# Optimization experiments

Measured on AMD Instinct MI355X. Metric: run time of the kernel, lower is better.

Reference implementation:

```python
import jax, jax.numpy as jnp
import numpy as np
from jax import lax

DIM = 256
POS = 32
RATIO = 4
LN_EPS = 1e-5


def _layernorm(x, g, b):
    m = x.mean(-1, keepdims=True)
    v = ((x - m) ** 2).mean(-1, keepdims=True)
    return (x - m) * lax.rsqrt(v + LN_EPS) * g + b


def _pos_embed(pos, h, w):
    # pos: [1, C, POS, POS] -> bilinear (align_corners=False / half-pixel) -> [1, h*w, C]
    p = jax.image.resize(pos, (1, pos.shape[1], h, w), method='bilinear')
    return p.transpose(0, 2, 3, 1).reshape(1, h * w, pos.shape[1])


def _scan_branch(u, ln_g, ln_b, Wf, bf, Ww, bw, Wo, bo):
    # u: [B, N, C]. Pooled LN context -> concat gates -> gated linear recurrence.
    c = _layernorm(u.mean(1), ln_g, ln_b)                       # [B, C]
    z = jnp.concatenate([u, jnp.broadcast_to(c[:, None, :], u.shape)], -1)
    d = jax.nn.softplus(z @ Wf + bf)
    g = jax.nn.sigmoid(z @ Ww + bw)
    o = jax.nn.sigmoid(z @ Wo + bo)
    a = jnp.exp(-d)
    b = (1.0 - a) * (g * u)

    def step(s, t):
        a_t, b_t, o_t, u_t = t
        s = a_t * s + b_t
        return s, o_t * s + (1.0 - o_t) * u_t

    xs = tuple(jnp.swapaxes(v, 0, 1) for v in (a, b, o, u))     # [N, B, C]
    s0 = jnp.zeros((u.shape[0], u.shape[2]), u.dtype)
    _, y = lax.scan(step, s0, xs)
    return jnp.swapaxes(y, 0, 1)                                # [B, N, C]


def setup_inputs() -> dict:
    key = jax.random.key(0)
    ks = jax.random.split(key, 32)
    d = DIM

    def W(k, i, o, s=0.02):
        return (jax.random.normal(k, (i, o), jnp.float32) * s)

    inp = {
        'x': jax.random.normal(ks[0], (8, d, 64, 64), jnp.float32),
        'Wt': W(ks[1], d, d), 'bt': jnp.zeros((d,), jnp.float32),
        'pos_fine': jax.random.normal(ks[2], (1, d, POS, POS), jnp.float32) * 0.02,
        'pos_glob': jax.random.normal(ks[3], (1, d, POS, POS), jnp.float32) * 0.02,
        'ln_g': jnp.ones((d,), jnp.float32), 'ln_b': jnp.zeros((d,), jnp.float32),
        'Wf': W(ks[4], 2 * d, d), 'bf': jnp.zeros((d,), jnp.float32),
        'Ww': W(ks[5], 2 * d, d), 'bw': jnp.zeros((d,), jnp.float32),
        'Wo': W(ks[6], 2 * d, d), 'bo': jnp.zeros((d,), jnp.float32),
        'Wr': W(ks[7], 3 * d, d), 'br': jnp.zeros((d,), jnp.float32),
        'Wgi': W(ks[8], 3 * d, d), 'bgi': jnp.zeros((d,), jnp.float32),
        'dw_w': jax.random.normal(ks[9], (d, 1, 3, 3), jnp.float32) * 0.1,
        'dw_b': jnp.zeros((d,), jnp.float32),
        'Wl': W(ks[10], d, d), 'bl': jnp.zeros((d,), jnp.float32),
        'Wlf': W(ks[11], 2 * d, d), 'blf': jnp.zeros((d,), jnp.float32),
        'Wout': W(ks[12], d, d), 'bout': jnp.zeros((d,), jnp.float32),
    }
    return inp


def reference(x, Wt, bt, pos_fine, pos_glob, ln_g, ln_b, Wf, bf, Ww, bw, Wo, bo,
              Wr, br, Wgi, bgi, dw_w, dw_b, Wl, bl, Wlf, blf, Wout, bout):
    bsz, c, h, w = x.shape
    gate_params = (ln_g, ln_b, Wf, bf, Ww, bw, Wo, bo)

    # fine sequence: token proj + interpolated learnable pos
    seq = x.transpose(0, 2, 3, 1).reshape(bsz, h * w, c)
    u = seq @ Wt + bt + _pos_embed(pos_fine, h, w)

    # bidirectional gated scan
    y_f = _scan_branch(u, *gate_params)
    y_b = jnp.flip(_scan_branch(jnp.flip(u, 1), *gate_params), 1)
    rho = jax.nn.sigmoid(jnp.concatenate([u, y_f, y_b], -1) @ Wr + br)
    y = rho * y_f + (1.0 - rho) * y_b

    # global branch: exact avg pool (H,W divisible by RATIO) -> scan -> upsample
    gh, gw = h // RATIO, w // RATIO
    x_g = x.reshape(bsz, c, gh, RATIO, gw, RATIO).mean((3, 5))
    seq_g = x_g.transpose(0, 2, 3, 1).reshape(bsz, gh * gw, c)
    u_g = seq_g @ Wt + bt + _pos_embed(pos_glob, gh, gw)
    y_g = _scan_branch(u_g, *gate_params)
    y_g_map = y_g.reshape(bsz, gh, gw, c).transpose(0, 3, 1, 2)
    y_g_up = jax.image.resize(y_g_map, (bsz, c, h, w), method='bilinear')
    y_g_seq = y_g_up.transpose(0, 2, 3, 1).reshape(bsz, h * w, c)

    lam = jax.nn.sigmoid(jnp.concatenate([y, y_g_seq, u], -1) @ Wgi + bgi)
    z = y + lam * y_g_seq

    # local depthwise conv branch
    v_map = lax.conv_general_dilated(x, dw_w, (1, 1), 'SAME',
                                     feature_group_count=c) + dw_b[None, :, None, None]
    v = v_map.transpose(0, 2, 3, 1).reshape(bsz, h * w, c) @ Wl + bl
    eta = jax.nn.sigmoid(jnp.concatenate([v, z], -1) @ Wlf + blf)
    u_out = eta * v + (1.0 - eta) * z

    # 1x1 conv output proj + residual
    out_map = (u_out @ Wout + bout).reshape(bsz, h, w, c).transpose(0, 3, 1, 2)
    return x + out_map
```

## Files before the change

kernel.cpp:

```cpp
#include <hip/hip_runtime.h>
#include <cstddef>

#define B_  8
#define C_  256
#define H_  64
#define W_  64
#define HW_ 4096
#define NG_ 256

typedef unsigned short u16;
typedef __attribute__((ext_vector_type(8))) short short8;
typedef __attribute__((ext_vector_type(4))) float f32x4;

__device__ __forceinline__ float sigm(float v) { return 1.f / (1.f + expf(-v)); }

__device__ __forceinline__ u16 f2bf(float f) {
    union { float f; unsigned u; } x; x.f = f;
    unsigned r = x.u + 0x7fff + ((x.u >> 16) & 1);
    return (u16)(r >> 16);
}
__device__ __forceinline__ float bf2f(u16 h) {
    union { unsigned u; float f; } x; x.u = ((unsigned)h) << 16;
    return x.f;
}

__global__ __launch_bounds__(256) void prepw_k(
    const float* __restrict__ Wt, const float* __restrict__ Wf, const float* __restrict__ Ww,
    const float* __restrict__ Wo, const float* __restrict__ Wr, const float* __restrict__ Wgi,
    const float* __restrict__ Wl, const float* __restrict__ Wlf, const float* __restrict__ Wout,
    u16* __restrict__ Wpre)
{
    int s = blockIdx.z;
    const float* Wsrc; int rowoff = 0;
    switch (s) {
        case 0: Wsrc = Wt; break;
        case 1: Wsrc = Wf; break;
        case 2: Wsrc = Ww; break;
        case 3: Wsrc = Wo; break;
        case 4: case 5: case 6: Wsrc = Wr;  rowoff = (s - 4) * 256; break;
        case 7: case 8: case 9: Wsrc = Wgi; rowoff = (s - 7) * 256; break;
        case 10: Wsrc = Wl; break;
        case 11: case 12: Wsrc = Wlf; rowoff = (s - 11) * 256; break;
        default: Wsrc = Wout; break;
    }
    __shared__ float t[32][33];
    int k0 = blockIdx.y * 32, n0 = blockIdx.x * 32;
    int tx = threadIdx.x, ty = threadIdx.y;
#pragma unroll
    for (int i = 0; i < 32; i += 8)
        t[ty + i][tx] = Wsrc[(size_t)(rowoff + k0 + ty + i) * 256 + n0 + tx];
    __syncthreads();
    u16* op = Wpre + (size_t)s * 65536;
#pragma unroll
    for (int i = 0; i < 32; i += 8)
        op[(size_t)(n0 + ty + i) * 256 + k0 + tx] = f2bf(t[tx][ty + i]);
}

#define SWZ(row, qoff) ((row) * 128 + ((qoff) ^ (((row) & 7) << 4)))

__global__ __launch_bounds__(256, 4) void gemm_bf16(
    const u16* __restrict__ A0, const u16* __restrict__ A1, const u16* __restrict__ A2,
    int nseg, const u16* __restrict__ Wpre, const float* __restrict__ bias,
    const float* __restrict__ pos, const float* __restrict__ aux0,
    const u16* __restrict__ auxb0, const u16* __restrict__ auxb1,
    float* __restrict__ out, u16* __restrict__ out2, int NTOK, int mode)
{
    __shared__ u16 Asm[64 * 64];
    __shared__ u16 Bsm[128 * 64];
    const int tid = threadIdx.x;
    const int lane = tid & 63, wave = tid >> 6;
    const int wm = wave & 1, wn = wave >> 1;
    const int m0 = blockIdx.x * 64, n0 = blockIdx.y * 128;
    const int l15 = lane & 15, lq = lane >> 4;

    f32x4 acc[2][4] = {};

    const int rowS = tid >> 3, colS = tid & 7;

    short8 av[2], bv[4];
    {
        av[0] = *(const short8*)(A0 + (size_t)(m0 + rowS) * 256 + colS * 8);
        av[1] = *(const short8*)(A0 + (size_t)(m0 + 32 + rowS) * 256 + colS * 8);
#pragma unroll
        for (int i = 0; i < 4; ++i)
            bv[i] = *(const short8*)(Wpre + (size_t)(n0 + i * 32 + rowS) * 256 + colS * 8);
    }

    const int nq = nseg * 4;
    for (int q = 0; q < nq; ++q) {
        __syncthreads();
        *(short8*)((char*)Asm + SWZ(rowS,      colS * 16)) = av[0];
        *(short8*)((char*)Asm + SWZ(rowS + 32, colS * 16)) = av[1];
#pragma unroll
        for (int i = 0; i < 4; ++i)
            *(short8*)((char*)Bsm + SWZ(i * 32 + rowS, colS * 16)) = bv[i];

        if (q + 1 < nq) {
            const int q1 = q + 1, seg = q1 >> 2, k0 = (q1 & 3) << 6;
            const u16* __restrict__ A = (seg == 0) ? A0 : ((seg == 1) ? A1 : A2);
            const u16* __restrict__ Wq = Wpre + (size_t)seg * 65536;
            av[0] = *(const short8*)(A + (size_t)(m0 + rowS) * 256 + k0 + colS * 8);
            av[1] = *(const short8*)(A + (size_t)(m0 + 32 + rowS) * 256 + k0 + colS * 8);
#pragma unroll
            for (int i = 0; i < 4; ++i)
                bv[i] = *(const short8*)(Wq + (size_t)(n0 + i * 32 + rowS) * 256 + k0 + colS * 8);
        }
        __syncthreads();

#pragma unroll
        for (int ks = 0; ks < 2; ++ks) {
            short8 af[2], bfr[4];
#pragma unroll
            for (int i = 0; i < 2; ++i) {
                const int row = wm * 32 + i * 16 + l15;
                af[i] = *(const short8*)((char*)Asm + SWZ(row, ks * 64 + lq * 16));
            }
#pragma unroll
            for (int j = 0; j < 4; ++j) {
                const int row = wn * 64 + j * 16 + l15;
                bfr[j] = *(const short8*)((char*)Bsm + SWZ(row, ks * 64 + lq * 16));
            }
#pragma unroll
            for (int i = 0; i < 2; ++i)
#pragma unroll
                for (int j = 0; j < 4; ++j)
                    acc[i][j] = __builtin_amdgcn_mfma_f32_16x16x32_bf16(
                        af[i], bfr[j], acc[i][j], 0, 0, 0);
        }
    }

#pragma unroll
    for (int i = 0; i < 2; ++i) {
        int mbase = m0 + wm * 32 + i * 16 + lq * 4;
#pragma unroll
        for (int j = 0; j < 4; ++j) {
            int n = n0 + wn * 64 + j * 16 + l15;
            if (mode == 9) {
                int b9 = mbase >> 12, hw = mbase & 4095;
                size_t oi = ((size_t)b9 * 256 + n) * 4096 + hw;
                float bn = bias[n];
                float4 xr = *(const float4*)(aux0 + oi);
                float4 res;
                res.x = xr.x + acc[i][j][0] + bn;
                res.y = xr.y + acc[i][j][1] + bn;
                res.z = xr.z + acc[i][j][2] + bn;
                res.w = xr.w + acc[i][j][3] + bn;
                *(float4*)(out + oi) = res;
                continue;
            }
            float bn = bias[n];
#pragma unroll
            for (int r = 0; r < 4; ++r) {
                int m = mbase + r;
                size_t idx = (size_t)m * 256 + n;
                float D = acc[i][j][r] + bn;
                if (mode == 1) {
                    float v = D + pos[(size_t)(m % NTOK) * 256 + n];
                    out[idx] = v; out2[idx] = f2bf(v);
                } else if (mode == 10) {
                    float v = D + pos[(size_t)(m % NTOK) * 256 + n];
                    out2[idx] = f2bf(v);
                } else if (mode == 11) {
                    float r_ = sigm(D);
                    out2[idx] = f2bf(r_ * bf2f(auxb0[idx]) + (1.f - r_) * bf2f(auxb1[idx]));
                } else if (mode == 6) {
                    float l = sigm(D);
                    out2[idx] = f2bf(bf2f(auxb1[idx]) + l * bf2f(auxb0[idx]));
                } else if (mode == 7) {
                    out2[idx] = f2bf(D);
                } else {
                    float e = sigm(D);
                    out2[idx] = f2bf(e * bf2f(auxb0[idx]) + (1.f - e) * bf2f(auxb1[idx]));
                }
            }
        }
    }
}

#define LDK 72
__global__ __launch_bounds__(256, 4) void gemm_gates3(
    const u16* __restrict__ A0, const u16* __restrict__ Wg, const float* __restrict__ cf,
    const u16* __restrict__ ubf, float* __restrict__ aF, float* __restrict__ bbF,
    u16* __restrict__ obf, int NTOK)
{
    __shared__ u16 Asm[64 * LDK];
    __shared__ u16 Bsm3[3][64 * LDK];
    const int tid = threadIdx.x;
    const int lane = tid & 63, wave = tid >> 6;
    const int wm = wave & 1, wn = wave >> 1;
    const int m0 = blockIdx.x * 64, n0 = blockIdx.y * 64;
    const int l15 = lane & 15, lq = lane >> 4;

    f32x4 acc[3][2][2] = {};

    const int rowA = tid >> 2, kA = (tid & 3) * 16;
    const u16* arow = A0 + (size_t)(m0 + rowA) * 256 + kA;
    const u16* wrow = Wg + (size_t)(n0 + rowA) * 256 + kA;

    for (int k0 = 0; k0 < 256; k0 += 64) {
        *(short8*)(&Asm[rowA * LDK + kA])     = *(const short8*)(arow + k0);
        *(short8*)(&Asm[rowA * LDK + kA + 8]) = *(const short8*)(arow + k0 + 8);
#pragma unroll
        for (int ws = 0; ws < 3; ++ws) {
            const u16* wr = wrow + (size_t)ws * 65536 + k0;
            *(short8*)(&Bsm3[ws][rowA * LDK + kA])     = *(const short8*)(wr);
            *(short8*)(&Bsm3[ws][rowA * LDK + kA + 8]) = *(const short8*)(wr + 8);
        }
        __syncthreads();
#pragma unroll
        for (int ks = 0; ks < 2; ++ks) {
            short8 af[2];
#pragma unroll
            for (int i = 0; i < 2; ++i)
                af[i] = *(const short8*)(&Asm[(wm * 32 + i * 16 + l15) * LDK + ks * 32 + lq * 8]);
#pragma unroll
            for (int ws = 0; ws < 3; ++ws) {
                short8 bfr[2];
#pragma unroll
                for (int j = 0; j < 2; ++j)
                    bfr[j] = *(const short8*)(&Bsm3[ws][(wn * 32 + j * 16 + l15) * LDK + ks * 32 + lq * 8]);
#pragma unroll
                for (int i = 0; i < 2; ++i)
#pragma unroll
                    for (int j = 0; j < 2; ++j)
                        acc[ws][i][j] = __builtin_amdgcn_mfma_f32_16x16x32_bf16(
                            af[i], bfr[j], acc[ws][i][j], 0, 0, 0);
            }
        }
        __syncthreads();
    }

#pragma unroll
    for (int i = 0; i < 2; ++i) {
        int mbase = m0 + wm * 32 + i * 16 + lq * 4;
        int bt_ = mbase / NTOK;
#pragma unroll
        for (int j = 0; j < 2; ++j) {
            int n = n0 + wn * 32 + j * 16 + l15;
            float cD = cf[((size_t)0 * B_ + bt_) * C_ + n];
            float cW = cf[((size_t)1 * B_ + bt_) * C_ + n];
            float cO = cf[((size_t)2 * B_ + bt_) * C_ + n];
#pragma unroll
            for (int r = 0; r < 4; ++r) {
                size_t idx = (size_t)(mbase + r) * 256 + n;
                float a_ = sigm(-(acc[0][i][j][r] + cD));
                float g_ = sigm(acc[1][i][j][r] + cW);
                float o_ = sigm(acc[2][i][j][r] + cO);
                float u_ = bf2f(ubf[idx]);
                aF[idx]  = a_;
                bbF[idx] = (1.f - a_) * g_ * u_;
                obf[idx] = f2bf(o_);
            }
        }
    }
}

__global__ __launch_bounds__(256) void transpose_bf_k(const float* __restrict__ in,
                                                      u16* __restrict__ outb)
{
    __shared__ float t[32][33];
    int b = blockIdx.z;
    int r0 = blockIdx.y * 32, c0 = blockIdx.x * 32;
    int tx = threadIdx.x, ty = threadIdx.y;
    const float* ip = in + (size_t)b * HW_ * C_;
    u16* op = outb + (size_t)b * HW_ * C_;
#pragma unroll
    for (int k = 0; k < 32; k += 8)
        t[ty + k][tx] = ip[(size_t)(r0 + ty + k) * HW_ + c0 + tx];
    __syncthreads();
#pragma unroll
    for (int k = 0; k < 32; k += 8)
        op[(size_t)(c0 + ty + k) * C_ + r0 + tx] = f2bf(t[tx][ty + k]);
}

__global__ __launch_bounds__(256) void dwconvt3_k(const float* __restrict__ x,
                                                  const float* __restrict__ dww,
                                                  const float* __restrict__ dwb,
                                                  u16* __restrict__ vseq)
{
    __shared__ float sx[32 * 384];
    __shared__ float sw[32 * 9];
    __shared__ float sb[32];
    const int t = threadIdx.x;
    const int l   = (blockIdx.x & 7) * 128 + (blockIdx.x >> 3);
    const int hch = l & 15;
    const int chb = (l >> 4) & 7;
    const int b   = l >> 7;
    const int r0 = chb * 32, h0 = hch * 4;

    for (int p = t; p < 288; p += 256) sw[p] = dww[(size_t)(r0 + p / 9) * 9 + p % 9];
    if (t < 32) sb[t] = dwb[r0 + t];

    const float* xb = x + (size_t)(b * 256 + r0) * 4096;
#pragma unroll
    for (int j = 0; j < 12; ++j) {
        int seg = j * 256 + t;
        int ch  = seg / 96;
        int r4  = seg - ch * 96;
        int rr  = r4 >> 4;
        int w4  = (r4 & 15) * 4;
        int hh  = h0 - 1 + rr;
        float4 v = make_float4(0.f, 0.f, 0.f, 0.f);
        if (hh >= 0 && hh <= 63)
            v = *(const float4*)(xb + (size_t)ch * 4096 + hh * 64 + w4);
        *(float4*)(&sx[seg * 4]) = v;
    }
    __syncthreads();

    const int w = t & 63, chq = t >> 6;
    float res[4][8];
#pragma unroll
    for (int i = 0; i < 8; ++i) {
        const int ch = chq * 8 + i;
        const float* cw = &sw[ch * 9];
        const float* bp = &sx[ch * 384 + w];
        float aa[4];
        aa[0] = aa[1] = aa[2] = aa[3] = sb[ch];
#pragma unroll
        for (int rr = 0; rr < 6; ++rr) {
            const float* rp = bp + rr * 64;
            float cc = rp[0];
            float lf = (w > 0)  ? rp[-1] : 0.f;
            float rt = (w < 63) ? rp[1]  : 0.f;
            if (rr < 4)            aa[rr]     += lf * cw[0] + cc * cw[1] + rt * cw[2];
            if (rr >= 1 && rr < 5) aa[rr - 1] += lf * cw[3] + cc * cw[4] + rt * cw[5];
            if (rr >= 2)           aa[rr - 2] += lf * cw[6] + cc * cw[7] + rt * cw[8];
        }
#pragma unroll
        for (int r = 0; r < 4; ++r) res[r][i] = aa[r];
    }

    size_t obase = ((size_t)b * HW_ + (size_t)(h0 * 64 + w)) * 256 + r0 + chq * 8;
#pragma unroll
    for (int r = 0; r < 4; ++r) {
        short8 v;
#pragma unroll
        for (int i = 0; i < 8; ++i) v[i] = (short)f2bf(res[r][i]);
        *(short8*)(vseq + obase + (size_t)r * 64 * 256) = v;
    }
}

__global__ __launch_bounds__(256) void pool_k(const float* __restrict__ x, u16* __restrict__ seqg)
{
    int b = blockIdx.x, c = blockIdx.y, ghw = threadIdx.x;
    int gh = ghw >> 4, gw = ghw & 15;
    const float* xp = x + ((size_t)b * C_ + c) * HW_;
    float s = 0.f;
#pragma unroll
    for (int dy = 0; dy < 4; ++dy)
#pragma unroll
        for (int dx = 0; dx < 4; ++dx)
            s += xp[(gh * 4 + dy) * W_ + gw * 4 + dx];
    seqg[((size_t)b * NG_ + ghw) * C_ + c] = f2bf(s * (1.f / 16.f));
}

__global__ __launch_bounds__(256) void posfine_k(const float* __restrict__ pf, float* __restrict__ posF)
{
    int hw = blockIdx.x, c = threadIdx.x;
    int h = hw >> 6, w = hw & 63;
    float fy = h * 0.5f - 0.25f, fx = w * 0.5f - 0.25f;
    int y0 = (int)floorf(fy); float wy = fy - (float)y0;
    int x0 = (int)floorf(fx); float wx = fx - (float)x0;
    int y0c = min(max(y0, 0), 31), y1c = min(max(y0 + 1, 0), 31);
    int x0c = min(max(x0, 0), 31), x1c = min(max(x0 + 1, 0), 31);
    const float* p = pf + (size_t)c * 1024;
    float v = (1.f - wy) * ((1.f - wx) * p[y0c * 32 + x0c] + wx * p[y0c * 32 + x1c])
            +        wy  * ((1.f - wx) * p[y1c * 32 + x0c] + wx * p[y1c * 32 + x1c]);
    posF[(size_t)hw * C_ + c] = v;
}

__global__ __launch_bounds__(256) void posglob_k(const float* __restrict__ pg, float* __restrict__ posG)
{
    int ghw = blockIdx.x, c = threadIdx.x;
    int gh = ghw >> 4, gw = ghw & 15;
    const float wt[4] = {0.125f, 0.375f, 0.375f, 0.125f};
    float wy[4], wx[4]; int jy[4], jx[4];
    float sy = 0.f, sx = 0.f;
#pragma unroll
    for (int k = 0; k < 4; ++k) {
        jy[k] = 2 * gh - 1 + k; jx[k] = 2 * gw - 1 + k;
        wy[k] = (jy[k] >= 0 && jy[k] < 32) ? wt[k] : 0.f; sy += wy[k];
        wx[k] = (jx[k] >= 0 && jx[k] < 32) ? wt[k] : 0.f; sx += wx[k];
    }
    const float* p = pg + (size_t)c * 1024;
    float acc = 0.f;
#pragma unroll
    for (int ky = 0; ky < 4; ++ky) {
        if (wy[ky] == 0.f) continue;
        float row = 0.f;
#pragma unroll
        for (int kx = 0; kx < 4; ++kx)
            if (wx[kx] != 0.f) row += wx[kx] * p[jy[ky] * 32 + jx[kx]];
        acc += wy[ky] * row;
    }
    posG[(size_t)ghw * C_ + c] = acc / (sy * sx);
}

__global__ __launch_bounds__(256) void upsample_k(const float* __restrict__ yg, u16* __restrict__ ygs)
{
    int b = blockIdx.x >> 12, hw = blockIdx.x & 4095, c = threadIdx.x;
    int h = hw >> 6, w = hw & 63;
    float fy = h * 0.25f - 0.375f, fx = w * 0.25f - 0.375f;
    int y0 = (int)floorf(fy); float wy = fy - (float)y0;
    int x0 = (int)floorf(fx); float wx = fx - (float)x0;
    int y0c = min(max(y0, 0), 15), y1c = min(max(y0 + 1, 0), 15);
    int x0c = min(max(x0, 0), 15), x1c = min(max(x0 + 1, 0), 15);
    const float* p = yg + (size_t)b * NG_ * C_ + c;
    float v = (1.f - wy) * ((1.f - wx) * p[(y0c * 16 + x0c) * C_] + wx * p[(y0c * 16 + x1c) * C_])
            +        wy  * ((1.f - wx) * p[(y1c * 16 + x0c) * C_] + wx * p[(y1c * 16 + x1c) * C_]);
    ygs[((size_t)b * HW_ + hw) * C_ + c] = f2bf(v);
}

__global__ __launch_bounds__(256) void meanpart_k(const float* __restrict__ u, float* __restrict__ part,
                                                  int Ntok, int chunkLen)
{
    int b = blockIdx.x, s = blockIdx.y, c = threadIdx.x;
    float acc = 0.f;
    for (int i = 0; i < chunkLen; ++i) {
        int t = s * chunkLen + i;
        acc += u[((size_t)b * Ntok + t) * C_ + c];
    }
    part[((size_t)b * gridDim.y + s) * C_ + c] = acc;
}

__global__ __launch_bounds__(256) void meanpart_bf_k(const u16* __restrict__ u, float* __restrict__ part,
                                                     int Ntok, int chunkLen)
{
    int b = blockIdx.x, s = blockIdx.y, c = threadIdx.x;
    float acc = 0.f;
    for (int i = 0; i < chunkLen; ++i) {
        int t = s * chunkLen + i;
        acc += bf2f(u[((size_t)b * Ntok + t) * C_ + c]);
    }
    part[((size_t)b * gridDim.y + s) * C_ + c] = acc;
}

__global__ __launch_bounds__(256) void ln_k(const float* __restrict__ part, int S, float invN,
                                            const float* __restrict__ g, const float* __restrict__ bta,
                                            float* __restrict__ cout)
{
    __shared__ float red[256];
    int c = threadIdx.x, b = blockIdx.x;
    float v = 0.f;
    for (int s = 0; s < S; ++s) v += part[((size_t)b * S + s) * C_ + c];
    v *= invN;
    red[c] = v; __syncthreads();
    for (int st = 128; st > 0; st >>= 1) { if (c < st) red[c] += red[c + st]; __syncthreads(); }
    float m = red[0] * (1.f / 256.f);
    __syncthreads();
    float d = v - m;
    red[c] = d * d; __syncthreads();
    for (int st = 128; st > 0; st >>= 1) { if (c < st) red[c] += red[c + st]; __syncthreads(); }
    float var = red[0] * (1.f / 256.f);
    cout[(size_t)b * C_ + c] = d * rsqrtf(var + 1e-5f) * g[c] + bta[c];
}

__global__ __launch_bounds__(256) void gatebias_k(const float* __restrict__ cvec,
    const float* __restrict__ Wf, const float* __restrict__ bf,
    const float* __restrict__ Ww, const float* __restrict__ bw,
    const float* __restrict__ Wo, const float* __restrict__ bo,
    float* __restrict__ outb)
{
    int n = threadIdx.x, b = blockIdx.x, gate = blockIdx.y;
    const float* Wm = (gate == 0) ? Wf : ((gate == 1) ? Ww : Wo);
    const float* bi = (gate == 0) ? bf : ((gate == 1) ? bw : bo);
    __shared__ float cs[256];
    cs[n] = cvec[(size_t)b * C_ + n];
    __syncthreads();
    float acc = bi[n];
    for (int k = 0; k < 256; ++k)
        acc += cs[k] * Wm[(size_t)(256 + k) * C_ + n];
    outb[((size_t)gate * B_ + b) * C_ + n] = acc;
}

__global__ __launch_bounds__(256) void scan_p1b(
    const float* __restrict__ a, const float* __restrict__ bb,
    float* __restrict__ AbF, float* __restrict__ BbF,
    float* __restrict__ AbB, float* __restrict__ BbB,
    int Ntok, int nchunk, int both)
{
    int c = threadIdx.x;
    int ch = blockIdx.x % nchunk;
    int b = blockIdx.x / nchunk;
    int CL = Ntok / nchunk;
    size_t base = ((size_t)b * Ntok + (size_t)ch * CL) * C_ + c;
    float sA = 1.f, sB = 0.f;
    for (int i = 0; i < CL; ++i) {
        float av = a[base + (size_t)i * C_];
        sB = av * sB + bb[base + (size_t)i * C_];
        sA *= av;
    }
    size_t o = ((size_t)b * nchunk + ch) * C_ + c;
    AbF[o] = sA; BbF[o] = sB;
    if (both) {
        sA = 1.f; sB = 0.f;
        for (int i = CL - 1; i >= 0; --i) {
            float av = a[base + (size_t)i * C_];
            sB = av * sB + bb[base + (size_t)i * C_];
            sA *= av;
        }
        size_t ob = ((size_t)b * nchunk + (nchunk - 1 - ch)) * C_ + c;
        AbB[ob] = sA; BbB[ob] = sB;
    }
}

__global__ __launch_bounds__(512) void scan_p2c(
    const float* __restrict__ AbF, const float* __restrict__ BbF, float* __restrict__ SbF,
    const float* __restrict__ AbB, const float* __restrict__ BbB, float* __restrict__ SbB,
    int nchunk, int both)
{
    const int c = threadIdx.x & 255, half = threadIdx.x >> 8, b = blockIdx.x;
    if (half && !both) return;
    const float* __restrict__ Ap = half ? AbB : AbF;
    const float* __restrict__ Bp = half ? BbB : BbF;
    float* __restrict__       Sp = half ? SbB : SbF;
    const size_t base = (size_t)b * nchunk * C_ + c;
    float a0[8], b0[8], a1[8], b1[8];
#pragma unroll
    for (int j = 0; j < 8; ++j) {
        a0[j] = Ap[base + (size_t)j * C_];
        b0[j] = Bp[base + (size_t)j * C_];
    }
    float s = 0.f;
    const int nb = nchunk >> 3;
    for (int t = 0; t < nb; ++t) {
        const size_t nbase = base + (size_t)(t + 1) * 8 * C_;
        if (t + 1 < nb) {
#pragma unroll
            for (int j = 0; j < 8; ++j) {
                a1[j] = Ap[nbase + (size_t)j * C_];
                b1[j] = Bp[nbase + (size_t)j * C_];
            }
        }
        const size_t cbase = base + (size_t)t * 8 * C_;
#pragma unroll
        for (int j = 0; j < 8; ++j) {
            Sp[cbase + (size_t)j * C_] = s;
            s = a0[j] * s + b0[j];
        }
#pragma unroll
        for (int j = 0; j < 8; ++j) { a0[j] = a1[j]; b0[j] = b1[j]; }
    }
}

__global__ __launch_bounds__(256) void scan_p3b(
    const float* __restrict__ a, const float* __restrict__ bb,
    const u16* __restrict__ obf, const u16* __restrict__ ubf,
    const float* __restrict__ SbF, const float* __restrict__ SbB,
    float* __restrict__ yout, u16* __restrict__ ybfF, u16* __restrict__ ybfB,
    int Ntok, int nchunk, int both)
{
    int c = threadIdx.x;
    int ch = blockIdx.x % nchunk;
    int b = blockIdx.x / nchunk;
    int CL = Ntok / nchunk;
    size_t base = ((size_t)b * Ntok + (size_t)ch * CL) * C_ + c;
    float s = SbF[((size_t)b * nchunk + ch) * C_ + c];
    for (int i = 0; i < CL; ++i) {
        size_t idx = base + (size_t)i * C_;
        float av = a[idx];
        s = av * s + bb[idx];
        float ov = bf2f(obf[idx]);
        float y = ov * s + (1.f - ov) * bf2f(ubf[idx]);
        if (yout) yout[idx] = y;
        if (ybfF) ybfF[idx] = f2bf(y);
    }
    if (both) {
        float sb = SbB[((size_t)b * nchunk + (nchunk - 1 - ch)) * C_ + c];
        for (int i = CL - 1; i >= 0; --i) {
            size_t idx = base + (size_t)i * C_;
            float av = a[idx];
            sb = av * sb + bb[idx];
            float ov = bf2f(obf[idx]);
            ybfB[idx] = f2bf(ov * sb + (1.f - ov) * bf2f(ubf[idx]));
        }
    }
}

extern "C" void kernel_launch(void* const* d_in, const int* in_sizes, int n_in,
                              void* d_out, int out_size, void* d_ws, size_t ws_size,
                              hipStream_t stream)
{
    const float* x        = (const float*)d_in[0];
    const float* Wt       = (const float*)d_in[1];
    const float* bt       = (const float*)d_in[2];
    const float* pos_fine = (const float*)d_in[3];
    const float* pos_glob = (const float*)d_in[4];
    const float* ln_g     = (const float*)d_in[5];
    const float* ln_b     = (const float*)d_in[6];
    const float* Wf       = (const float*)d_in[7];
    const float* bf       = (const float*)d_in[8];
    const float* Ww       = (const float*)d_in[9];
    const float* bw       = (const float*)d_in[10];
    const float* Wo       = (const float*)d_in[11];
    const float* bo       = (const float*)d_in[12];
    const float* Wr       = (const float*)d_in[13];
    const float* br       = (const float*)d_in[14];
    const float* Wgi      = (const float*)d_in[15];
    const float* bgi      = (const float*)d_in[16];
    const float* dww      = (const float*)d_in[17];
    const float* dwb      = (const float*)d_in[18];
    const float* Wl       = (const float*)d_in[19];
    const float* bl       = (const float*)d_in[20];
    const float* Wlf      = (const float*)d_in[21];
    const float* blf      = (const float*)d_in[22];
    const float* Wout     = (const float*)d_in[23];
    const float* bout     = (const float*)d_in[24];
    float* out = (float*)d_out;

    float* w = (float*)d_ws;
    const size_t BNC = (size_t)B_ * HW_ * C_;
    float* bu  = w + 0 * BNC;
    float* ba  = w + 1 * BNC;
    float* bbb = w + 2 * BNC;
    float* bo_ = w + 3 * BNC;
    u16* bf1 = (u16*)(w + 4 * BNC);
    u16* bf2 = bf1 + BNC;
    u16* bf3 = bf2 + BNC;
    u16* bf4 = bf3 + BNC;
    u16* bf5 = bf4 + BNC;
    float* ext = w + 4 * BNC + 5 * (BNC / 2);
    float* posF = ext;  ext += (size_t)HW_ * C_;
    float* posG = ext;  ext += (size_t)NG_ * C_;
    float* part = ext;  ext += (size_t)B_ * 32 * C_;
    float* cln  = ext;  ext += (size_t)B_ * C_;
    float* cf   = ext;  ext += (size_t)3 * B_ * C_;
    float* ug   = ext;  ext += (size_t)B_ * NG_ * C_;
    float* ag   = ext;  ext += (size_t)B_ * NG_ * C_;
    float* bbg  = ext;  ext += (size_t)B_ * NG_ * C_;
    float* ygt  = ext;  ext += (size_t)B_ * NG_ * C_;
    u16* seqg_bf = (u16*)ext;  ext += (size_t)B_ * NG_ * C_ / 2;
    u16* ug_bf   = (u16*)ext;  ext += (size_t)B_ * NG_ * C_ / 2;
    u16* og_bf   = (u16*)ext;  ext += (size_t)B_ * NG_ * C_ / 2;
    u16* Wpre    = (u16*)ext;
    const size_t CHS = (size_t)B_ * 256 * C_;
    float* chAF = bu + 0 * CHS;
    float* chBF = bu + 1 * CHS;
    float* chSF = bu + 2 * CHS;
    float* chAB = bu + 3 * CHS;
    float* chBB = bu + 4 * CHS;
    float* chSB = bu + 5 * CHS;
    u16* obf    = (u16*)bo_;

    const dim3 blk256(256);
    const dim3 blkT(32, 8);
    const dim3 gBig(B_ * HW_ / 64, 2);
    const dim3 gSml(B_ * NG_ / 64, 2);
    const dim3 gGateF(B_ * HW_ / 64, 4);
    const dim3 gGateG(B_ * NG_ / 64, 4);
    const size_t WS = 65536;
    const int NCH_F = 256;
    const int NCH_G = 16;
    const float *F0 = nullptr; const u16 *U0 = nullptr;
    float *FW = nullptr; u16 *UW = nullptr;

    prepw_k<<<dim3(8, 8, 14), blkT, 0, stream>>>(Wt, Wf, Ww, Wo, Wr, Wgi, Wl, Wlf, Wout, Wpre);

    transpose_bf_k<<<dim3(HW_ / 32, C_ / 32, B_), blkT, 0, stream>>>(x, bf1);
    posfine_k<<<HW_, blk256, 0, stream>>>(pos_fine, posF);
    gemm_bf16<<<gBig, blk256, 0, stream>>>(bf1, U0, U0, 1, Wpre + 0 * WS, bt,
        posF, F0, U0, U0, FW, bf2, HW_, 10);

    pool_k<<<dim3(B_, C_), blk256, 0, stream>>>(x, seqg_bf);
    posglob_k<<<NG_, blk256, 0, stream>>>(pos_glob, posG);
    gemm_bf16<<<gSml, blk256, 0, stream>>>(seqg_bf, U0, U0, 1, Wpre + 0 * WS, bt,
        posG, F0, U0, U0, ug, ug_bf, NG_, 1);
    meanpart_k<<<dim3(B_, 8), blk256, 0, stream>>>(ug, part, NG_, 32);
    ln_k<<<B_, blk256, 0, stream>>>(part, 8, 1.f / NG_, ln_g, ln_b, cln);
    gatebias_k<<<dim3(B_, 3), blk256, 0, stream>>>(cln, Wf, bf, Ww, bw, Wo, bo, cf);
    gemm_gates3<<<gGateG, blk256, 0, stream>>>(ug_bf, Wpre + 1 * WS, cf, ug_bf,
        ag, bbg, og_bf, NG_);
    scan_p1b<<<B_ * NCH_G, blk256, 0, stream>>>(ag, bbg, chAF, chBF, FW, FW, NG_, NCH_G, 0);
    scan_p2c<<<B_, dim3(512), 0, stream>>>(chAF, chBF, chSF, F0, F0, FW, NCH_G, 0);
    scan_p3b<<<B_ * NCH_G, blk256, 0, stream>>>(ag, bbg, og_bf, ug_bf, chSF, F0,
        ygt, UW, UW, NG_, NCH_G, 0);
    upsample_k<<<B_ * HW_, blk256, 0, stream>>>(ygt, bf5);

    meanpart_bf_k<<<dim3(B_, 32), blk256, 0, stream>>>(bf2, part, HW_, 128);
    ln_k<<<B_, blk256, 0, stream>>>(part, 32, 1.f / HW_, ln_g, ln_b, cln);
    gatebias_k<<<dim3(B_, 3), blk256, 0, stream>>>(cln, Wf, bf, Ww, bw, Wo, bo, cf);
    gemm_gates3<<<gGateF, blk256, 0, stream>>>(bf2, Wpre + 1 * WS, cf, bf2,
        ba, bbb, obf, HW_);
    scan_p1b<<<B_ * NCH_F, blk256, 0, stream>>>(ba, bbb, chAF, chBF, chAB, chBB, HW_, NCH_F, 1);
    scan_p2c<<<B_, dim3(512), 0, stream>>>(chAF, chBF, chSF, chAB, chBB, chSB, NCH_F, 1);
    scan_p3b<<<B_ * NCH_F, blk256, 0, stream>>>(ba, bbb, obf, bf2, chSF, chSB,
        FW, bf1, bf3, HW_, NCH_F, 1);

    gemm_bf16<<<gBig, blk256, 0, stream>>>(bf2, bf1, bf3, 3, Wpre + 4 * WS, br,
        F0, F0, bf1, bf3, FW, bf4, HW_, 11);

    gemm_bf16<<<gBig, blk256, 0, stream>>>(bf4, bf5, bf2, 3, Wpre + 7 * WS, bgi,
        F0, F0, bf5, bf4, FW, bf1, HW_, 6);

    dwconvt3_k<<<dim3(1024), blk256, 0, stream>>>(x, dww, dwb, bf3);
    gemm_bf16<<<gBig, blk256, 0, stream>>>(bf3, U0, U0, 1, Wpre + 10 * WS, bl,
        F0, F0, U0, U0, FW, bf2, HW_, 7);
    gemm_bf16<<<gBig, blk256, 0, stream>>>(bf2, bf1, U0, 2, Wpre + 11 * WS, blf,
        F0, F0, bf2, bf1, FW, bf3, HW_, 8);

    gemm_bf16<<<gBig, blk256, 0, stream>>>(bf3, U0, U0, 1, Wpre + 13 * WS, bout,
        F0, x, U0, U0, out, UW, HW_, 9);
}
```

Baseline: 568.4 us.

## Fuse chunk-scan phase 1 into gates GEMM epilogue and swizzle LDS tiles

The first pass of the chunked scan, which computed per-chunk (A,B) summaries, is folded into the gates GEMM epilogue. Each 16-row tile is reduced with a register prefix and lane shuffles, for both forward and backward directions, so the separate scan_p1b kernel and its re-read of a/b from global memory go away. The GEMM's shared-memory staging also switches from padded rows to a swizzled layout, with register prefetch of the next k-slice. This assumes 16-token chunks (NCH = NTOK/16), which must match what scan_p2c/p3b expect, and it adds shuffle work to the epilogue.

```diff
diff --git a/kernel.cpp b/kernel.cpp
--- a/kernel.cpp
+++ b/kernel.cpp
@@ -177,14 +177,16 @@
     }
 }
 
-#define LDK 72
 __global__ __launch_bounds__(256, 4) void gemm_gates3(
     const u16* __restrict__ A0, const u16* __restrict__ Wg, const float* __restrict__ cf,
     const u16* __restrict__ ubf, float* __restrict__ aF, float* __restrict__ bbF,
-    u16* __restrict__ obf, int NTOK)
-{
-    __shared__ u16 Asm[64 * LDK];
-    __shared__ u16 Bsm3[3][64 * LDK];
+    u16* __restrict__ obf,
+    float* __restrict__ chAF, float* __restrict__ chBF,
+    float* __restrict__ chAB, float* __restrict__ chBB,
+    int NTOK, int both)
+{
+    __shared__ u16 Asm[64 * 64];
+    __shared__ u16 Bsm3[3][64 * 64];
     const int tid = threadIdx.x;
     const int lane = tid & 63, wave = tid >> 6;
     const int wm = wave & 1, wn = wave >> 1;
@@ -193,32 +195,58 @@
 
     f32x4 acc[3][2][2] = {};
 
-    const int rowA = tid >> 2, kA = (tid & 3) * 16;
-    const u16* arow = A0 + (size_t)(m0 + rowA) * 256 + kA;
-    const u16* wrow = Wg + (size_t)(n0 + rowA) * 256 + kA;
-
-    for (int k0 = 0; k0 < 256; k0 += 64) {
-        *(short8*)(&Asm[rowA * LDK + kA])     = *(const short8*)(arow + k0);
-        *(short8*)(&Asm[rowA * LDK + kA + 8]) = *(const short8*)(arow + k0 + 8);
+    const int rowS = tid >> 3, colS = tid & 7;
+
+    short8 av[2], bv[3][2];
+    {
+        av[0] = *(const short8*)(A0 + (size_t)(m0 + rowS) * 256 + colS * 8);
+        av[1] = *(const short8*)(A0 + (size_t)(m0 + 32 + rowS) * 256 + colS * 8);
 #pragma unroll
         for (int ws = 0; ws < 3; ++ws) {
-            const u16* wr = wrow + (size_t)ws * 65536 + k0;
-            *(short8*)(&Bsm3[ws][rowA * LDK + kA])     = *(const short8*)(wr);
-            *(short8*)(&Bsm3[ws][rowA * LDK + kA + 8]) = *(const short8*)(wr + 8);
-        }
+            const u16* wp = Wg + (size_t)ws * 65536;
+            bv[ws][0] = *(const short8*)(wp + (size_t)(n0 + rowS) * 256 + colS * 8);
+            bv[ws][1] = *(const short8*)(wp + (size_t)(n0 + 32 + rowS) * 256 + colS * 8);
+        }
+    }
+
+    for (int q = 0; q < 4; ++q) {
         __syncthreads();
+        *(short8*)((char*)Asm + SWZ(rowS,      colS * 16)) = av[0];
+        *(short8*)((char*)Asm + SWZ(rowS + 32, colS * 16)) = av[1];
+#pragma unroll
+        for (int ws = 0; ws < 3; ++ws) {
+            *(short8*)((char*)Bsm3[ws] + SWZ(rowS,      colS * 16)) = bv[ws][0];
+            *(short8*)((char*)Bsm3[ws] + SWZ(rowS + 32, colS * 16)) = bv[ws][1];
+        }
+        if (q < 3) {
+            const int k0 = (q + 1) << 6;
+            av[0] = *(const short8*)(A0 + (size_t)(m0 + rowS) * 256 + k0 + colS * 8);
+            av[1] = *(const short8*)(A0 + (size_t)(m0 + 32 + rowS) * 256 + k0 + colS * 8);
+#pragma unroll
+            for (int ws = 0; ws < 3; ++ws) {
+                const u16* wp = Wg + (size_t)ws * 65536;
+                bv[ws][0] = *(const short8*)(wp + (size_t)(n0 + rowS) * 256 + k0 + colS * 8);
+                bv[ws][1] = *(const short8*)(wp + (size_t)(n0 + 32 + rowS) * 256 + k0 + colS * 8);
+            }
+        }
+        __syncthreads();
+
 #pragma unroll
         for (int ks = 0; ks < 2; ++ks) {
             short8 af[2];
 #pragma unroll
-            for (int i = 0; i < 2; ++i)
-                af[i] = *(const short8*)(&Asm[(wm * 32 + i * 16 + l15) * LDK + ks * 32 + lq * 8]);
+            for (int i = 0; i < 2; ++i) {
+                const int row = wm * 32 + i * 16 + l15;
+                af[i] = *(const short8*)((char*)Asm + SWZ(row, ks * 64 + lq * 16));
+            }
 #pragma unroll
             for (int ws = 0; ws < 3; ++ws) {
                 short8 bfr[2];
 #pragma unroll
-                for (int j = 0; j < 2; ++j)
-                    bfr[j] = *(const short8*)(&Bsm3[ws][(wn * 32 + j * 16 + l15) * LDK + ks * 32 + lq * 8]);
+                for (int j = 0; j < 2; ++j) {
+                    const int row = wn * 32 + j * 16 + l15;
+                    bfr[j] = *(const short8*)((char*)Bsm3[ws] + SWZ(row, ks * 64 + lq * 16));
+                }
 #pragma unroll
                 for (int i = 0; i < 2; ++i)
 #pragma unroll
@@ -227,19 +255,21 @@
                             af[i], bfr[j], acc[ws][i][j], 0, 0, 0);
             }
         }
-        __syncthreads();
-    }
-
+    }
+
+    const int nch = NTOK >> 4;
 #pragma unroll
     for (int i = 0; i < 2; ++i) {
-        int mbase = m0 + wm * 32 + i * 16 + lq * 4;
-        int bt_ = mbase / NTOK;
+        const int mtile = m0 + wm * 32 + i * 16;
+        const int mbase = mtile + lq * 4;
+        const int bt_ = mbase / NTOK;
 #pragma unroll
         for (int j = 0; j < 2; ++j) {
             int n = n0 + wn * 32 + j * 16 + l15;
             float cD = cf[((size_t)0 * B_ + bt_) * C_ + n];
             float cW = cf[((size_t)1 * B_ + bt_) * C_ + n];
             float cO = cf[((size_t)2 * B_ + bt_) * C_ + n];
+            float a4[4], b4[4];
 #pragma unroll
             for (int r = 0; r < 4; ++r) {
                 size_t idx = (size_t)(mbase + r) * 256 + n;
@@ -247,9 +277,48 @@
                 float g_ = sigm(acc[1][i][j][r] + cW);
                 float o_ = sigm(acc[2][i][j][r] + cO);
                 float u_ = bf2f(ubf[idx]);
+                float b_ = (1.f - a_) * g_ * u_;
                 aF[idx]  = a_;
-                bbF[idx] = (1.f - a_) * g_ * u_;
+                bbF[idx] = b_;
                 obf[idx] = f2bf(o_);
+                a4[r] = a_; b4[r] = b_;
+            }
+            float A = 1.f, Bv = 0.f;
+#pragma unroll
+            for (int r = 0; r < 4; ++r) { Bv = a4[r] * Bv + b4[r]; A *= a4[r]; }
+            {
+                float Ao = __shfl_xor(A, 16), Bo = __shfl_xor(Bv, 16);
+                if ((lq & 1) == 0) { Bv = Ao * Bv + Bo; A = Ao * A; }
+                else               { Bv = A * Bo + Bv;  A = A * Ao; }
+            }
+            {
+                float Ao = __shfl_xor(A, 32), Bo = __shfl_xor(Bv, 32);
+                if ((lq & 2) == 0) { Bv = Ao * Bv + Bo; A = Ao * A; }
+                else               { Bv = A * Bo + Bv;  A = A * Ao; }
+            }
+            if (lq == 0) {
+                size_t ci = (size_t)(mtile >> 4) * C_ + n;
+                chAF[ci] = A; chBF[ci] = Bv;
+            }
+            if (both) {
+                float Ab = 1.f, Bb = 0.f;
+#pragma unroll
+                for (int r = 3; r >= 0; --r) { Bb = a4[r] * Bb + b4[r]; Ab *= a4[r]; }
+                {
+                    float Ao = __shfl_xor(Ab, 16), Bo = __shfl_xor(Bb, 16);
+                    if ((lq & 1) == 0) { Bb = Ab * Bo + Bb; Ab = Ab * Ao; }
+                    else               { Bb = Ao * Bb + Bo; Ab = Ao * Ab; }
+                }
+                {
+                    float Ao = __shfl_xor(Ab, 32), Bo = __shfl_xor(Bb, 32);
+                    if ((lq & 2) == 0) { Bb = Ab * Bo + Bb; Ab = Ab * Ao; }
+                    else               { Bb = Ao * Bb + Bo; Ab = Ao * Ab; }
+                }
+                if (lq == 0) {
+                    int ch = (mtile % NTOK) >> 4;
+                    size_t cir = ((size_t)bt_ * nch + (nch - 1 - ch)) * C_ + n;
+                    chAB[cir] = Ab; chBB[cir] = Bb;
+                }
             }
         }
     }
@@ -471,37 +540,6 @@
     for (int k = 0; k < 256; ++k)
         acc += cs[k] * Wm[(size_t)(256 + k) * C_ + n];
     outb[((size_t)gate * B_ + b) * C_ + n] = acc;
-}
-
-__global__ __launch_bounds__(256) void scan_p1b(
-    const float* __restrict__ a, const float* __restrict__ bb,
-    float* __restrict__ AbF, float* __restrict__ BbF,
-    float* __restrict__ AbB, float* __restrict__ BbB,
-    int Ntok, int nchunk, int both)
-{
-    int c = threadIdx.x;
-    int ch = blockIdx.x % nchunk;
-    int b = blockIdx.x / nchunk;
-    int CL = Ntok / nchunk;
-    size_t base = ((size_t)b * Ntok + (size_t)ch * CL) * C_ + c;
-    float sA = 1.f, sB = 0.f;
-    for (int i = 0; i < CL; ++i) {
-        float av = a[base + (size_t)i * C_];
-        sB = av * sB + bb[base + (size_t)i * C_];
-        sA *= av;
-    }
-    size_t o = ((size_t)b * nchunk + ch) * C_ + c;
-    AbF[o] = sA; BbF[o] = sB;
-    if (both) {
-        sA = 1.f; sB = 0.f;
-        for (int i = CL - 1; i >= 0; --i) {
-            float av = a[base + (size_t)i * C_];
-            sB = av * sB + bb[base + (size_t)i * C_];
-            sA *= av;
-        }
-        size_t ob = ((size_t)b * nchunk + (nchunk - 1 - ch)) * C_ + c;
-        AbB[ob] = sA; BbB[ob] = sB;
-    }
 }
 
 __global__ __launch_bounds__(512) void scan_p2c(
@@ -669,8 +707,7 @@
     ln_k<<<B_, blk256, 0, stream>>>(part, 8, 1.f / NG_, ln_g, ln_b, cln);
     gatebias_k<<<dim3(B_, 3), blk256, 0, stream>>>(cln, Wf, bf, Ww, bw, Wo, bo, cf);
     gemm_gates3<<<gGateG, blk256, 0, stream>>>(ug_bf, Wpre + 1 * WS, cf, ug_bf,
-        ag, bbg, og_bf, NG_);
-    scan_p1b<<<B_ * NCH_G, blk256, 0, stream>>>(ag, bbg, chAF, chBF, FW, FW, NG_, NCH_G, 0);
+        ag, bbg, og_bf, chAF, chBF, FW, FW, NG_, 0);
     scan_p2c<<<B_, dim3(512), 0, stream>>>(chAF, chBF, chSF, F0, F0, FW, NCH_G, 0);
     scan_p3b<<<B_ * NCH_G, blk256, 0, stream>>>(ag, bbg, og_bf, ug_bf, chSF, F0,
         ygt, UW, UW, NG_, NCH_G, 0);
@@ -680,8 +717,7 @@
     ln_k<<<B_, blk256, 0, stream>>>(part, 32, 1.f / HW_, ln_g, ln_b, cln);
     gatebias_k<<<dim3(B_, 3), blk256, 0, stream>>>(cln, Wf, bf, Ww, bw, Wo, bo, cf);
     gemm_gates3<<<gGateF, blk256, 0, stream>>>(bf2, Wpre + 1 * WS, cf, bf2,
-        ba, bbb, obf, HW_);
-    scan_p1b<<<B_ * NCH_F, blk256, 0, stream>>>(ba, bbb, chAF, chBF, chAB, chBB, HW_, NCH_F, 1);
+        ba, bbb, obf, chAF, chBF, chAB, chBB, HW_, 1);
     scan_p2c<<<B_, dim3(512), 0, stream>>>(chAF, chBF, chSF, chAB, chBB, chSB, NCH_F, 1);
     scan_p3b<<<B_ * NCH_F, blk256, 0, stream>>>(ba, bbb, obf, bf2, chSF, chSB,
         FW, bf1, bf3, HW_, NCH_F, 1);
```

Measured after the change: 552.6 us. 2.8% less time.
